# Kernel tuning notes

Hardware: AMD Instinct MI355X
Metric: run time of the kernel (lower is better)

## Reference

```python
import jax, jax.numpy as jnp
import numpy as np


def setup_inputs() -> dict:
    key = jax.random.key(0)
    k1, k2 = jax.random.split(key)
    x = jax.random.normal(k1, (8, 320, 320), dtype=jnp.float32)
    # flow displacements in pixels; scale a bit for realistic motion magnitude
    u = jax.random.normal(k2, (8, 12, 320, 320, 2), dtype=jnp.float32) * 4.0
    return {"x": x, "u": u}


def _bilinear_warp(xf, uf):
    """xf: (P, M, N) images, uf: (P, M, N, 2) flow (u[...,0]=dx cols, u[...,1]=dy rows).
    out(i,j) = bilinear sample of xf at (i + dy, j + dx), zero outside image."""
    P, M, N = xf.shape
    jj = jnp.arange(N, dtype=uf.dtype)            # (N,)
    ii = jnp.arange(M, dtype=uf.dtype)[:, None]   # (M,1)
    sx = jj + uf[..., 0]                          # (P,M,N) sample column
    sy = ii + uf[..., 1]                          # (P,M,N) sample row
    x0 = jnp.floor(sx)
    y0 = jnp.floor(sy)
    wx = sx - x0
    wy = sy - y0
    x0i = x0.astype(jnp.int32)
    y0i = y0.astype(jnp.int32)
    flat = xf.reshape(P, M * N)

    def gather(yi, xi):
        valid = (xi >= 0) & (xi < N) & (yi >= 0) & (yi < M)
        idx = jnp.clip(yi, 0, M - 1) * N + jnp.clip(xi, 0, N - 1)
        v = jnp.take_along_axis(flat, idx.reshape(P, -1), axis=1).reshape(P, M, N)
        return jnp.where(valid, v, jnp.zeros((), xf.dtype))

    v00 = gather(y0i, x0i)
    v01 = gather(y0i, x0i + 1)
    v10 = gather(y0i + 1, x0i)
    v11 = gather(y0i + 1, x0i + 1)
    return (v00 * (1 - wx) * (1 - wy)
            + v01 * wx * (1 - wy)
            + v10 * (1 - wx) * wy
            + v11 * wx * wy)


def reference(x, u):
    F, M, N = u.shape[-4], u.shape[-3], u.shape[-2]
    lead = u.shape[:-4]
    # repeat_interleave(unsqueeze(x,-3), F, dim=-3) == broadcast x across frame dim
    xb = jnp.broadcast_to(jnp.expand_dims(x, -3), lead + (F, M, N)).reshape(-1, M, N)
    uf = u.reshape(-1, M, N, 2)
    out = _bilinear_warp(xb, uf)
    return out.reshape(u.shape[:-1])
```

## Files before the change

kernel.cpp:

```cpp
#include <hip/hip_runtime.h>

#define PP 8
#define FF 12
#define MM 320
#define NN 320
#define TILE 32
#define HALO 16
#define LW   (TILE + 2 * HALO)
#define PW   68
#define FPB  2

typedef float fvec4 __attribute__((ext_vector_type(4)));
typedef float fvec2 __attribute__((ext_vector_type(2)));

__global__ __launch_bounds__(512, 8) void warp_tile_kernel(
    const float* __restrict__ x,
    const float* __restrict__ u,
    float* __restrict__ out)
{
    __shared__ float tile[LW * PW];

    int zz = blockIdx.z;
    int p  = zz / (FF / FPB);
    int f0 = (zz % (FF / FPB)) * FPB;
    int i0 = blockIdx.y * TILE;
    int j0 = blockIdx.x * TILE;

    const float* __restrict__ img = x + p * (MM * NN);

#pragma unroll
    for (int it = 0; it < 2; ++it) {
        int idx = (int)threadIdx.x + it * 512;
        int r  = idx >> 4;
        int c4 = idx & 15;
        int gr = i0 - HALO + r;
        int gc = j0 - HALO + c4 * 4;
        fvec4 v = {0.0f, 0.0f, 0.0f, 0.0f};
        if ((unsigned)gr < MM && (unsigned)gc < NN)
            v = *(const fvec4*)(img + gr * NN + gc);
        *(fvec4*)&tile[r * PW + c4 * 4] = v;
    }
    __syncthreads();

    int tcol = ((int)threadIdx.x & 15) * 2;
    int row0 = ((int)threadIdx.x >> 4);
    int gi = i0 + row0;
    int gj = j0 + tcol;

#pragma unroll
    for (int ff = 0; ff < FPB; ++ff) {
        int pf = p * FF + (f0 + ff);
        const float* __restrict__ ubase = u + (size_t)pf * (MM * NN * 2);
        float* __restrict__ obase = out + (size_t)pf * (MM * NN);

        fvec4 ua = *(const fvec4*)(ubase + 2 * ((size_t)gi * NN + gj));
        float dx[2] = {ua.x, ua.z};
        float dy[2] = {ua.y, ua.w};

        float res[2];
#pragma unroll
        for (int k = 0; k < 2; ++k) {
            float sx = (float)(gj + k) + dx[k];
            float sy = (float)gi + dy[k];
            float fx0 = floorf(sx);
            float fy0 = floorf(sy);
            float wx = sx - fx0;
            float wy = sy - fy0;
            int x0i = (int)fx0;
            int y0i = (int)fy0;

            int lx = x0i - (j0 - HALO);
            int ly = y0i - (i0 - HALO);

            float v00, v01, v10, v11;
            if (((unsigned)lx < (LW - 1)) & ((unsigned)ly < (LW - 1))) {
                const float* t = &tile[ly * PW + lx];
                v00 = t[0];
                v01 = t[1];
                v10 = t[PW];
                v11 = t[PW + 1];
            } else {
                int xc0 = min(max(x0i,     0), NN - 1);
                int xc1 = min(max(x0i + 1, 0), NN - 1);
                int yc0 = min(max(y0i,     0), MM - 1);
                int yc1 = min(max(y0i + 1, 0), MM - 1);
                bool vx0 = (x0i >= 0)     & (x0i < NN);
                bool vx1 = (x0i + 1 >= 0) & (x0i + 1 < NN);
                bool vy0 = (y0i >= 0)     & (y0i < MM);
                bool vy1 = (y0i + 1 >= 0) & (y0i + 1 < MM);
                int r0i = yc0 * NN;
                int r1i = yc1 * NN;
                v00 = (vy0 & vx0) ? img[r0i + xc0] : 0.0f;
                v01 = (vy0 & vx1) ? img[r0i + xc1] : 0.0f;
                v10 = (vy1 & vx0) ? img[r1i + xc0] : 0.0f;
                v11 = (vy1 & vx1) ? img[r1i + xc1] : 0.0f;
            }

            float vt = fmaf(wx, v01 - v00, v00);
            float vb = fmaf(wx, v11 - v10, v10);
            res[k] = fmaf(wy, vb - vt, vt);
        }

        fvec2 o = {res[0], res[1]};
        __builtin_nontemporal_store(o, (fvec2*)(obase + (size_t)gi * NN + gj));
    }
}

extern "C" void kernel_launch(void* const* d_in, const int* in_sizes, int n_in,
                              void* d_out, int out_size, void* d_ws, size_t ws_size,
                              hipStream_t stream) {
    const float* x = (const float*)d_in[0];
    const float* u = (const float*)d_in[1];
    float* out = (float*)d_out;

    dim3 grid(NN / TILE, MM / TILE, PP * (FF / FPB));
    dim3 block(512);
    warp_tile_kernel<<<grid, block, 0, stream>>>(x, u, out);
}
```

Baseline: 128.5 us.

## Replace shared-memory halo tiles with a zero-padded image and direct cached gathers

```diff
diff --git a/kernel.cpp b/kernel.cpp
--- a/kernel.cpp
+++ b/kernel.cpp
@@ -4,105 +4,68 @@
 #define FF 12
 #define MM 320
 #define NN 320
-#define TILE 32
-#define HALO 16
-#define LW   (TILE + 2 * HALO)
-#define PW   68
-#define FPB  2
+#define PAD 32
+#define PM (MM + 2 * PAD)
+#define PN (NN + 2 * PAD)
 
 typedef float fvec4 __attribute__((ext_vector_type(4)));
 typedef float fvec2 __attribute__((ext_vector_type(2)));
 
-__global__ __launch_bounds__(512, 8) void warp_tile_kernel(
-    const float* __restrict__ x,
+__global__ __launch_bounds__(256) void pad_kernel(const float* __restrict__ x,
+                                                  float* __restrict__ xp)
+{
+    int lin = blockIdx.x * 256 + (int)threadIdx.x;
+    int p   = lin / (PM * PN / 4);
+    int rem = lin - p * (PM * PN / 4);
+    int r   = rem / (PN / 4);
+    int c   = (rem - r * (PN / 4)) * 4;
+    int sr  = r - PAD;
+    int sc  = c - PAD;
+    fvec4 v = {0.f, 0.f, 0.f, 0.f};
+    if ((unsigned)sr < MM && (unsigned)sc < NN)
+        v = *(const fvec4*)(x + (size_t)p * (MM * NN) + sr * NN + sc);
+    *(fvec4*)(xp + (size_t)p * (PM * PN) + r * PN + c) = v;
+}
+
+__global__ __launch_bounds__(320) void warp_gather_kernel(
+    const float* __restrict__ xp,
     const float* __restrict__ u,
     float* __restrict__ out)
 {
-    __shared__ float tile[LW * PW];
+    int j  = (int)threadIdx.x;
+    int i0 = blockIdx.x * 4;
+    int pf = blockIdx.y;
+    int p  = pf / FF;
 
-    int zz = blockIdx.z;
-    int p  = zz / (FF / FPB);
-    int f0 = (zz % (FF / FPB)) * FPB;
-    int i0 = blockIdx.y * TILE;
-    int j0 = blockIdx.x * TILE;
+    const float* __restrict__ img = xp  + (size_t)p  * (PM * PN);
+    const float* __restrict__ ub  = u   + (size_t)pf * (MM * NN * 2);
+    float* __restrict__ ob        = out + (size_t)pf * (MM * NN);
 
-    const float* __restrict__ img = x + p * (MM * NN);
-
+    float fj = (float)j;
 #pragma unroll
-    for (int it = 0; it < 2; ++it) {
-        int idx = (int)threadIdx.x + it * 512;
-        int r  = idx >> 4;
-        int c4 = idx & 15;
-        int gr = i0 - HALO + r;
-        int gc = j0 - HALO + c4 * 4;
-        fvec4 v = {0.0f, 0.0f, 0.0f, 0.0f};
-        if ((unsigned)gr < MM && (unsigned)gc < NN)
-            v = *(const fvec4*)(img + gr * NN + gc);
-        *(fvec4*)&tile[r * PW + c4 * 4] = v;
-    }
-    __syncthreads();
-
-    int tcol = ((int)threadIdx.x & 15) * 2;
-    int row0 = ((int)threadIdx.x >> 4);
-    int gi = i0 + row0;
-    int gj = j0 + tcol;
-
-#pragma unroll
-    for (int ff = 0; ff < FPB; ++ff) {
-        int pf = p * FF + (f0 + ff);
-        const float* __restrict__ ubase = u + (size_t)pf * (MM * NN * 2);
-        float* __restrict__ obase = out + (size_t)pf * (MM * NN);
-
-        fvec4 ua = *(const fvec4*)(ubase + 2 * ((size_t)gi * NN + gj));
-        float dx[2] = {ua.x, ua.z};
-        float dy[2] = {ua.y, ua.w};
-
-        float res[2];
-#pragma unroll
-        for (int k = 0; k < 2; ++k) {
-            float sx = (float)(gj + k) + dx[k];
-            float sy = (float)gi + dy[k];
-            float fx0 = floorf(sx);
-            float fy0 = floorf(sy);
-            float wx = sx - fx0;
-            float wy = sy - fy0;
-            int x0i = (int)fx0;
-            int y0i = (int)fy0;
-
-            int lx = x0i - (j0 - HALO);
-            int ly = y0i - (i0 - HALO);
-
-            float v00, v01, v10, v11;
-            if (((unsigned)lx < (LW - 1)) & ((unsigned)ly < (LW - 1))) {
-                const float* t = &tile[ly * PW + lx];
-                v00 = t[0];
-                v01 = t[1];
-                v10 = t[PW];
-                v11 = t[PW + 1];
-            } else {
-                int xc0 = min(max(x0i,     0), NN - 1);
-                int xc1 = min(max(x0i + 1, 0), NN - 1);
-                int yc0 = min(max(y0i,     0), MM - 1);
-                int yc1 = min(max(y0i + 1, 0), MM - 1);
-                bool vx0 = (x0i >= 0)     & (x0i < NN);
-                bool vx1 = (x0i + 1 >= 0) & (x0i + 1 < NN);
-                bool vy0 = (y0i >= 0)     & (y0i < MM);
-                bool vy1 = (y0i + 1 >= 0) & (y0i + 1 < MM);
-                int r0i = yc0 * NN;
-                int r1i = yc1 * NN;
-                v00 = (vy0 & vx0) ? img[r0i + xc0] : 0.0f;
-                v01 = (vy0 & vx1) ? img[r0i + xc1] : 0.0f;
-                v10 = (vy1 & vx0) ? img[r1i + xc0] : 0.0f;
-                v11 = (vy1 & vx1) ? img[r1i + xc1] : 0.0f;
-            }
-
-            float vt = fmaf(wx, v01 - v00, v00);
-            float vb = fmaf(wx, v11 - v10, v10);
-            res[k] = fmaf(wy, vb - vt, vt);
-        }
-
-        fvec2 o = {res[0], res[1]};
-        __builtin_nontemporal_store(o, (fvec2*)(obase + (size_t)gi * NN + gj));
+    for (int r = 0; r < 4; ++r) {
+        int i = i0 + r;
+        fvec2 uv = __builtin_nontemporal_load(
+            (const fvec2*)(ub + 2 * ((size_t)i * NN + j)));
+        float sx = fj + uv.x;
+        float sy = (float)i + uv.y;
+        float fx0 = floorf(sx);
+        float fy0 = floorf(sy);
+        float wx = sx - fx0;
+        float wy = sy - fy0;
+        int xq = (int)fx0 + PAD;
+        int yq = (int)fy0 + PAD;
+        xq = min(max(xq, 0), PN - 2);
+        yq = min(max(yq, 0), PM - 2);
+        const float* c00 = img + yq * PN + xq;
+        float v00 = c00[0];
+        float v01 = c00[1];
+        float v10 = c00[PN];
+        float v11 = c00[PN + 1];
+        float vt = fmaf(wx, v01 - v00, v00);
+        float vb = fmaf(wx, v11 - v10, v10);
+        float res = fmaf(wy, vb - vt, vt);
+        __builtin_nontemporal_store(res, ob + (size_t)i * NN + j);
     }
 }
 
@@ -112,8 +75,11 @@
     const float* x = (const float*)d_in[0];
     const float* u = (const float*)d_in[1];
     float* out = (float*)d_out;
+    float* xp  = (float*)d_ws;
 
-    dim3 grid(NN / TILE, MM / TILE, PP * (FF / FPB));
-    dim3 block(512);
-    warp_tile_kernel<<<grid, block, 0, stream>>>(x, u, out);
+    dim3 pgrid((PP * PM * PN / 4) / 256);
+    pad_kernel<<<pgrid, dim3(256), 0, stream>>>(x, xp);
+
+    dim3 ggrid(MM / 4, PP * FF);
+    warp_gather_kernel<<<ggrid, dim3(320), 0, stream>>>(xp, u, out);
 }
```

After: 143.0 us. +11.2%, slower.

## Enlarge tiles and frames per block to amortize halo loads across frames

Applied to the files above, without the earlier changes.

```diff
diff --git a/kernel.cpp b/kernel.cpp
--- a/kernel.cpp
+++ b/kernel.cpp
@@ -4,35 +4,32 @@
 #define FF 12
 #define MM 320
 #define NN 320
-#define TILE 32
+#define TILE 40
 #define HALO 16
 #define LW   (TILE + 2 * HALO)
-#define PW   68
-#define FPB  2
+#define PW   76
+#define FPB  6
 
 typedef float fvec4 __attribute__((ext_vector_type(4)));
 typedef float fvec2 __attribute__((ext_vector_type(2)));
 
-__global__ __launch_bounds__(512, 8) void warp_tile_kernel(
+__global__ __launch_bounds__(320, 5) void warp_tile_kernel(
     const float* __restrict__ x,
     const float* __restrict__ u,
     float* __restrict__ out)
 {
     __shared__ float tile[LW * PW];
 
-    int zz = blockIdx.z;
-    int p  = zz / (FF / FPB);
-    int f0 = (zz % (FF / FPB)) * FPB;
+    int p  = blockIdx.z >> 1;
+    int f0 = (blockIdx.z & 1) * FPB;
     int i0 = blockIdx.y * TILE;
     int j0 = blockIdx.x * TILE;
 
     const float* __restrict__ img = x + p * (MM * NN);
 
-#pragma unroll
-    for (int it = 0; it < 2; ++it) {
-        int idx = (int)threadIdx.x + it * 512;
-        int r  = idx >> 4;
-        int c4 = idx & 15;
+    for (int idx = (int)threadIdx.x; idx < LW * (LW / 4); idx += 320) {
+        int r  = idx / 18;
+        int c4 = idx - r * 18;
         int gr = i0 - HALO + r;
         int gc = j0 - HALO + c4 * 4;
         fvec4 v = {0.0f, 0.0f, 0.0f, 0.0f};
@@ -42,20 +39,25 @@
     }
     __syncthreads();
 
-    int tcol = ((int)threadIdx.x & 15) * 2;
-    int row0 = ((int)threadIdx.x >> 4);
-    int gi = i0 + row0;
-    int gj = j0 + tcol;
+    int pf0 = p * FF + f0;
 
-#pragma unroll
-    for (int ff = 0; ff < FPB; ++ff) {
-        int pf = p * FF + (f0 + ff);
-        const float* __restrict__ ubase = u + (size_t)pf * (MM * NN * 2);
-        float* __restrict__ obase = out + (size_t)pf * (MM * NN);
+#pragma unroll 3
+    for (int it = 0; it < 15; ++it) {
+        int idx = (int)threadIdx.x + it * 320;
+        int f   = idx / 800;
+        int pr  = idx - f * 800;
+        int row = pr / 20;
+        int cp  = pr - row * 20;
+        int gi = i0 + row;
+        int gj = j0 + 2 * cp;
 
-        fvec4 ua = *(const fvec4*)(ubase + 2 * ((size_t)gi * NN + gj));
-        float dx[2] = {ua.x, ua.z};
-        float dy[2] = {ua.y, ua.w};
+        const float* __restrict__ ub = u + (size_t)(pf0 + f) * (MM * NN * 2);
+        float* __restrict__ ob = out + (size_t)(pf0 + f) * (MM * NN);
+
+        fvec4 uv = __builtin_nontemporal_load(
+            (const fvec4*)(ub + 2 * ((size_t)gi * NN + gj)));
+        float dx[2] = {uv.x, uv.z};
+        float dy[2] = {uv.y, uv.w};
 
         float res[2];
 #pragma unroll
@@ -102,7 +104,7 @@
         }
 
         fvec2 o = {res[0], res[1]};
-        __builtin_nontemporal_store(o, (fvec2*)(obase + (size_t)gi * NN + gj));
+        __builtin_nontemporal_store(o, (fvec2*)(ob + (size_t)gi * NN + gj));
     }
 }
 
@@ -114,6 +116,6 @@
     float* out = (float*)d_out;
 
     dim3 grid(NN / TILE, MM / TILE, PP * (FF / FPB));
-    dim3 block(512);
+    dim3 block(320);
     warp_tile_kernel<<<grid, block, 0, stream>>>(x, u, out);
 }
```

Result: slower. 146.6 us (+14.0%).
